# Optimization experiments

Measured on AMD Instinct MI355X. Metric: run time of the kernel, lower is better.

## Reference

```python
import jax, jax.numpy as jnp
import numpy as np

N_NODES = 50000
N_EDGES = 640000
HIDDEN = 128
NUM_GRAPHS = 50
EPS = 1e-5


def setup_inputs() -> dict:
    key = jax.random.key(0)
    k1, k2, k3, k4 = jax.random.split(key, 4)
    node = jax.random.normal(k1, (N_NODES, HIDDEN), dtype=jnp.float32)
    edge_index = jax.random.randint(k2, (2, N_EDGES), 0, N_NODES, dtype=jnp.int64)
    edge_attr = jax.random.uniform(k3, (N_EDGES,), dtype=jnp.float32)
    batch_ptr = jnp.sort(jax.random.randint(k4, (N_NODES,), 0, NUM_GRAPHS, dtype=jnp.int64))
    # GraphNorm learned params (init: weight=1, bias=0, mean_scale=1); perturb for a non-trivial test
    kw, kb, km = jax.random.split(jax.random.fold_in(key, 1), 3)
    weight = 1.0 + 0.1 * jax.random.normal(kw, (HIDDEN,), dtype=jnp.float32)
    bias = 0.1 * jax.random.normal(kb, (HIDDEN,), dtype=jnp.float32)
    mean_scale = 1.0 + 0.1 * jax.random.normal(km, (HIDDEN,), dtype=jnp.float32)
    return {"node": node, "edge_index": edge_index, "edge_attr": edge_attr,
            "batch_ptr": batch_ptr, "weight": weight, "bias": bias, "mean_scale": mean_scale}


def _segment_mean(x, seg, num_segments):
    s = jax.ops.segment_sum(x, seg, num_segments=num_segments)
    cnt = jax.ops.segment_sum(jnp.ones((x.shape[0], 1), x.dtype), seg, num_segments=num_segments)
    return s / jnp.maximum(cnt, 1.0)


def reference(node, edge_index, edge_attr, batch_ptr, weight, bias, mean_scale):
    n = node.shape[0]
    row, col = edge_index[0], edge_index[1]  # source -> target
    # gcn_norm (add_self_loops=False): symmetric normalization by target-degree
    deg = jax.ops.segment_sum(edge_attr, col, num_segments=n)
    dinv = jnp.where(deg > 0, deg ** -0.5, 0.0)
    norm_w = dinv[row] * edge_attr * dinv[col]  # [E]
    # LGConv propagate: scatter-add normalized source features to targets
    msg = node[row] * norm_w[:, None]            # [E, H]
    agg = jnp.zeros_like(node).at[col].add(msg)  # [N, H]
    # residual (skip_connection=True)
    h = node + agg
    # GraphNorm over per-graph segments
    mean = _segment_mean(h, batch_ptr, NUM_GRAPHS)            # [G, H]
    centered = h - mean[batch_ptr] * mean_scale               # [N, H]
    var = _segment_mean(centered * centered, batch_ptr, NUM_GRAPHS)
    out = centered / jnp.sqrt(var[batch_ptr] + EPS) * weight + bias
    return jax.nn.relu(out)
```

## Files before the change

kernel.cpp:

```cpp
#include <hip/hip_runtime.h>

#define N_NODES 50000
#define N_EDGES 640000
#define HIDDEN 128
#define NUM_GRAPHS 50
#define EPS 1e-5f
#define NBLK 196

#define CNT_SHIFT 44
#define FIX_MASK ((1ULL << CNT_SHIFT) - 1)
#define FIX_SCALE 4294967296.0f
#define FIX_INV (1.0f / 4294967296.0f)


__global__ void hist_kernel(const int* __restrict__ col, const float* __restrict__ ea,
                            unsigned long long* __restrict__ cnt64, int* __restrict__ rank) {
    int e = blockIdx.x * blockDim.x + threadIdx.x;
    if (e >= N_EDGES) return;
    int c = col[e];
    unsigned long long fx = (unsigned long long)(ea[e] * FIX_SCALE + 0.5f);
    unsigned long long old = atomicAdd(&cnt64[c], (1ULL << CNT_SHIFT) | fx);
    rank[e] = (int)(old >> CNT_SHIFT);
}

__global__ void scan1_kernel(const unsigned long long* __restrict__ cnt64,
                             int* __restrict__ bsum, float* __restrict__ dinv) {
    __shared__ int lds[256];
    int i = blockIdx.x * 256 + threadIdx.x;
    int c = 0;
    if (i < N_NODES) {
        unsigned long long v = cnt64[i];
        c = (int)(v >> CNT_SHIFT);
        unsigned long long lo = v & FIX_MASK;
        float deg = (float)lo * FIX_INV;
        dinv[i] = (lo != 0ULL) ? (1.0f / sqrtf(deg)) : 0.f;
    }
    lds[threadIdx.x] = c;
    __syncthreads();
    for (int off = 128; off > 0; off >>= 1) {
        if (threadIdx.x < off) lds[threadIdx.x] += lds[threadIdx.x + off];
        __syncthreads();
    }
    if (threadIdx.x == 0) bsum[blockIdx.x] = lds[0];
}

__global__ void scan2_kernel(const int* __restrict__ bsum, int* __restrict__ boff) {
    __shared__ int lds[256];
    int t = threadIdx.x;
    int v = (t < NBLK) ? bsum[t] : 0;
    lds[t] = v;
    __syncthreads();
    for (int off = 1; off < 256; off <<= 1) {
        int x = (t >= off) ? lds[t - off] : 0;
        __syncthreads();
        lds[t] += x;
        __syncthreads();
    }
    if (t < NBLK) boff[t] = lds[t] - v;
}

__global__ void scan3_kernel(const unsigned long long* __restrict__ cnt64,
                             const int* __restrict__ boff, int* __restrict__ rowptr) {
    __shared__ int lds[256];
    int i = blockIdx.x * 256 + threadIdx.x;
    int v = (i < N_NODES) ? (int)(cnt64[i] >> CNT_SHIFT) : 0;
    lds[threadIdx.x] = v;
    __syncthreads();
    for (int off = 1; off < 256; off <<= 1) {
        int x = (threadIdx.x >= off) ? lds[threadIdx.x - off] : 0;
        __syncthreads();
        lds[threadIdx.x] += x;
        __syncthreads();
    }
    if (i < N_NODES) rowptr[i] = boff[blockIdx.x] + lds[threadIdx.x] - v;
}

__global__ void place_kernel(const int* __restrict__ row, const int* __restrict__ col,
                             const float* __restrict__ ea, const float* __restrict__ rank,
                             const int* __restrict__ rowptr, const float* __restrict__ dinv,
                             int2* __restrict__ edat) {
    int e = blockIdx.x * blockDim.x + threadIdx.x;
    if (e >= N_EDGES) return;
    int r = row[e], c = col[e];
    float w = dinv[r] * ea[e];
    int pos = rowptr[c] + ((const int*)rank)[e];
    edat[pos] = make_int2(r, __float_as_int(w));
}

__global__ void gather_kernel(const int* __restrict__ rowptr,
                              const unsigned long long* __restrict__ cnt64,
                              const int2* __restrict__ edat, const float* __restrict__ dinv,
                              const float* __restrict__ node, float* __restrict__ out) {
    int n = blockIdx.x * 4 + (threadIdx.x >> 6);
    int lane = threadIdx.x & 63;
    if (n >= N_NODES) return;
    int j = rowptr[n];
    int end = j + (int)(cnt64[n] >> CNT_SHIFT);
    float dn = dinv[n];
    float2 a0 = {0.f, 0.f}, a1 = {0.f, 0.f}, a2 = {0.f, 0.f}, a3 = {0.f, 0.f};
    for (; j + 8 <= end; j += 8) {
        int2 e0 = edat[j + 0]; int2 e1 = edat[j + 1];
        int2 e2 = edat[j + 2]; int2 e3 = edat[j + 3];
        int2 e4 = edat[j + 4]; int2 e5 = edat[j + 5];
        int2 e6 = edat[j + 6]; int2 e7 = edat[j + 7];
        float2 v0 = ((const float2*)(node + (size_t)e0.x * HIDDEN))[lane];
        float2 v1 = ((const float2*)(node + (size_t)e1.x * HIDDEN))[lane];
        float2 v2 = ((const float2*)(node + (size_t)e2.x * HIDDEN))[lane];
        float2 v3 = ((const float2*)(node + (size_t)e3.x * HIDDEN))[lane];
        float2 v4 = ((const float2*)(node + (size_t)e4.x * HIDDEN))[lane];
        float2 v5 = ((const float2*)(node + (size_t)e5.x * HIDDEN))[lane];
        float2 v6 = ((const float2*)(node + (size_t)e6.x * HIDDEN))[lane];
        float2 v7 = ((const float2*)(node + (size_t)e7.x * HIDDEN))[lane];
        float w0 = __int_as_float(e0.y), w1 = __int_as_float(e1.y);
        float w2 = __int_as_float(e2.y), w3 = __int_as_float(e3.y);
        float w4 = __int_as_float(e4.y), w5 = __int_as_float(e5.y);
        float w6 = __int_as_float(e6.y), w7 = __int_as_float(e7.y);
        a0.x = fmaf(v0.x, w0, a0.x); a0.y = fmaf(v0.y, w0, a0.y);
        a1.x = fmaf(v1.x, w1, a1.x); a1.y = fmaf(v1.y, w1, a1.y);
        a2.x = fmaf(v2.x, w2, a2.x); a2.y = fmaf(v2.y, w2, a2.y);
        a3.x = fmaf(v3.x, w3, a3.x); a3.y = fmaf(v3.y, w3, a3.y);
        a0.x = fmaf(v4.x, w4, a0.x); a0.y = fmaf(v4.y, w4, a0.y);
        a1.x = fmaf(v5.x, w5, a1.x); a1.y = fmaf(v5.y, w5, a1.y);
        a2.x = fmaf(v6.x, w6, a2.x); a2.y = fmaf(v6.y, w6, a2.y);
        a3.x = fmaf(v7.x, w7, a3.x); a3.y = fmaf(v7.y, w7, a3.y);
    }
    for (; j < end; ++j) {
        int2 e = edat[j];
        float w = __int_as_float(e.y);
        float2 v = ((const float2*)(node + (size_t)e.x * HIDDEN))[lane];
        a0.x = fmaf(v.x, w, a0.x); a0.y = fmaf(v.y, w, a0.y);
    }
    float2 base = ((const float2*)(node + (size_t)n * HIDDEN))[lane];
    float sx = base.x + dn * ((a0.x + a1.x) + (a2.x + a3.x));
    float sy = base.y + dn * ((a0.y + a1.y) + (a2.y + a3.y));
    ((float2*)(out + (size_t)n * HIDDEN))[lane] = make_float2(sx, sy);
}


__global__ void stats_kernel(const float* __restrict__ h, const int* __restrict__ batch,
                             float* __restrict__ sum, float* __restrict__ sumsq) {
    int sub = threadIdx.x >> 5;
    int c4 = (threadIdx.x & 31) << 2;
    int i0 = blockIdx.x * 64;
    float4 s = make_float4(0.f, 0.f, 0.f, 0.f);
    float4 ss = make_float4(0.f, 0.f, 0.f, 0.f);
    int gcur = -1;
    for (int k = 0; k < 8; ++k) {
        int i = i0 + k * 8 + sub;
        if (i >= N_NODES) break;
        int g = batch[i];
        if (g != gcur) {
            if (gcur >= 0) {
                float* sp = &sum[gcur * HIDDEN + c4];
                atomicAdd(sp + 0, s.x); atomicAdd(sp + 1, s.y);
                atomicAdd(sp + 2, s.z); atomicAdd(sp + 3, s.w);
                float* qp = &sumsq[gcur * HIDDEN + c4];
                atomicAdd(qp + 0, ss.x); atomicAdd(qp + 1, ss.y);
                atomicAdd(qp + 2, ss.z); atomicAdd(qp + 3, ss.w);
            }
            gcur = g;
            s = make_float4(0.f, 0.f, 0.f, 0.f);
            ss = make_float4(0.f, 0.f, 0.f, 0.f);
        }
        float4 v = *(const float4*)(h + (size_t)i * HIDDEN + c4);
        s.x += v.x; s.y += v.y; s.z += v.z; s.w += v.w;
        ss.x += v.x * v.x; ss.y += v.y * v.y; ss.z += v.z * v.z; ss.w += v.w * v.w;
    }
    if (gcur >= 0) {
        float* sp = &sum[gcur * HIDDEN + c4];
        atomicAdd(sp + 0, s.x); atomicAdd(sp + 1, s.y);
        atomicAdd(sp + 2, s.z); atomicAdd(sp + 3, s.w);
        float* qp = &sumsq[gcur * HIDDEN + c4];
        atomicAdd(qp + 0, ss.x); atomicAdd(qp + 1, ss.y);
        atomicAdd(qp + 2, ss.z); atomicAdd(qp + 3, ss.w);
    }
}

__global__ void finalize_kernel(const float* __restrict__ sum, const float* __restrict__ sumsq,
                                const int* __restrict__ batch,
                                const float* __restrict__ mean_scale,
                                const float* __restrict__ weight,
                                float* __restrict__ msc, float* __restrict__ scale) {
    int t = blockIdx.x * blockDim.x + threadIdx.x;
    if (t >= NUM_GRAPHS * HIDDEN) return;
    int g = t >> 7;
    int c = t & 127;
    int lo0 = 0, hi0 = N_NODES;
    while (lo0 < hi0) { int m = (lo0 + hi0) >> 1; if (batch[m] < g) lo0 = m + 1; else hi0 = m; }
    int lo1 = lo0, hi1 = N_NODES;
    while (lo1 < hi1) { int m = (lo1 + hi1) >> 1; if (batch[m] < g + 1) lo1 = m + 1; else hi1 = m; }
    float n = fmaxf((float)(lo1 - lo0), 1.0f);
    float mean = sum[t] / n;
    float m2 = sumsq[t] / n;
    float ms = mean * mean_scale[c];
    float var = m2 - 2.f * ms * mean + ms * ms;
    msc[t] = ms;
    scale[t] = weight[c] / sqrtf(var + EPS);
}

__global__ void norm_kernel(float* __restrict__ out, const int* __restrict__ batch,
                            const float* __restrict__ msc, const float* __restrict__ scale,
                            const float* __restrict__ bias) {
    int t = blockIdx.x * blockDim.x + threadIdx.x;
    if (t >= N_NODES * HIDDEN / 4) return;
    int node_i = t >> 5;
    int c4 = (t & 31) << 2;
    int g = batch[node_i];
    float4 h = ((const float4*)out)[t];
    float4 m = *(const float4*)&msc[g * HIDDEN + c4];
    float4 sc = *(const float4*)&scale[g * HIDDEN + c4];
    float4 b = *(const float4*)&bias[c4];
    float4 o;
    o.x = fmaxf((h.x - m.x) * sc.x + b.x, 0.f);
    o.y = fmaxf((h.y - m.y) * sc.y + b.y, 0.f);
    o.z = fmaxf((h.z - m.z) * sc.z + b.z, 0.f);
    o.w = fmaxf((h.w - m.w) * sc.w + b.w, 0.f);
    ((float4*)out)[t] = o;
}


__global__ void deg_kernel(const int* __restrict__ col, const float* __restrict__ ea,
                           float* __restrict__ deg) {
    int e = blockIdx.x * blockDim.x + threadIdx.x;
    if (e < N_EDGES) atomicAdd(&deg[col[e]], ea[e]);
}

__global__ void dinv_kernel(float* __restrict__ deg) {
    int i = blockIdx.x * blockDim.x + threadIdx.x;
    if (i < N_NODES) {
        float d = deg[i];
        deg[i] = (d > 0.f) ? (1.0f / sqrtf(d)) : 0.f;
    }
}

__global__ void scatter_kernel(const int* __restrict__ row, const int* __restrict__ col,
                               const float* __restrict__ ea, const float* __restrict__ dinv,
                               const float* __restrict__ node, float* __restrict__ out) {
    int idx = blockIdx.x * blockDim.x + threadIdx.x;
    int e = idx >> 6;
    int lane = idx & 63;
    if (e >= N_EDGES) return;
    int r = row[e];
    int c = col[e];
    float w = dinv[r] * ea[e] * dinv[c];
    const float* src = node + (size_t)r * HIDDEN;
    float* dst = out + (size_t)c * HIDDEN;
    atomicAdd(&dst[lane], src[lane] * w);
    atomicAdd(&dst[lane + 64], src[lane + 64] * w);
}


extern "C" void kernel_launch(void* const* d_in, const int* in_sizes, int n_in,
                              void* d_out, int out_size, void* d_ws, size_t ws_size,
                              hipStream_t stream) {
    const float* node       = (const float*)d_in[0];
    const int*   eidx       = (const int*)d_in[1];
    const float* ea         = (const float*)d_in[2];
    const int*   batch      = (const int*)d_in[3];
    const float* weight     = (const float*)d_in[4];
    const float* bias       = (const float*)d_in[5];
    const float* mean_scale = (const float*)d_in[6];
    float* out = (float*)d_out;

    const int* row = eidx;
    const int* col = eidx + N_EDGES;

    char* wsb = (char*)d_ws;
    unsigned long long* cnt64 = (unsigned long long*)wsb;
    float* sum    = (float*)(cnt64 + 50048);
    float* sumsq  = sum + 6400;
    float* dinv   = sumsq + 6400;
    int*   rank   = (int*)(dinv + 50048);
    int*   rowptr = rank + N_EDGES;
    int2*  edat   = (int2*)(rowptr + 50048);
    float* msc    = (float*)(edat + N_EDGES);
    float* scale  = msc + 6400;
    int*   bsum   = (int*)(scale + 6400);
    int*   boff   = bsum + 256;
    size_t need = (size_t)((char*)(boff + 256) - wsb);

    if (ws_size >= need) {
        hipMemsetAsync(d_ws, 0, 50048 * 8 + 6400 * 2 * 4, stream);

        hist_kernel<<<(N_EDGES + 255) / 256, 256, 0, stream>>>(col, ea, cnt64, rank);
        scan1_kernel<<<NBLK, 256, 0, stream>>>(cnt64, bsum, dinv);
        scan2_kernel<<<1, 256, 0, stream>>>(bsum, boff);
        scan3_kernel<<<NBLK, 256, 0, stream>>>(cnt64, boff, rowptr);
        place_kernel<<<(N_EDGES + 255) / 256, 256, 0, stream>>>(
            row, col, ea, (const float*)rank, rowptr, dinv, edat);
        gather_kernel<<<(N_NODES + 3) / 4, 256, 0, stream>>>(
            rowptr, cnt64, edat, dinv, node, out);
    } else {
        float* f_deg   = (float*)wsb;
        float* f_sum   = f_deg + 50048;
        float* f_sumsq = f_sum + 6400;
        float* f_msc   = f_sumsq + 6400;
        float* f_scale = f_msc + 6400;
        sum = f_sum; sumsq = f_sumsq; msc = f_msc; scale = f_scale;

        hipMemsetAsync(d_ws, 0, (50048 + 6400 * 2) * sizeof(float), stream);
        hipMemcpyAsync(d_out, node, (size_t)N_NODES * HIDDEN * sizeof(float),
                       hipMemcpyDeviceToDevice, stream);
        deg_kernel<<<(N_EDGES + 255) / 256, 256, 0, stream>>>(col, ea, f_deg);
        dinv_kernel<<<(N_NODES + 255) / 256, 256, 0, stream>>>(f_deg);
        long long st = (long long)N_EDGES * 64;
        scatter_kernel<<<(int)((st + 255) / 256), 256, 0, stream>>>(row, col, ea, f_deg, node, out);
    }

    stats_kernel<<<(N_NODES + 63) / 64, 256, 0, stream>>>(out, batch, sum, sumsq);
    finalize_kernel<<<(NUM_GRAPHS * HIDDEN + 255) / 256, 256, 0, stream>>>(
        sum, sumsq, batch, mean_scale, weight, msc, scale);
    norm_kernel<<<(N_NODES * HIDDEN / 4 + 255) / 256, 256, 0, stream>>>(
        out, batch, msc, scale, bias);
}
```

Measured before the change: 255.7 us.

## Gather bf16 pre-scaled node features with padded CSR segments and merged scan

Adds a conversion kernel that pre-multiplies node features by dinv and packs them as bf16, so the gather reads half as many bytes per neighbour row. CSR segments are padded to multiples of 8 with zeroed slots, which removes the gather's scalar tail loop. The single-block scan2 kernel is folded into scan3. In exchange there is an extra full pass over node features, a larger memset of the padded edge buffer, and bf16 rounding error in the aggregated messages.

```diff
diff --git a/kernel.cpp b/kernel.cpp
--- a/kernel.cpp
+++ b/kernel.cpp
@@ -11,6 +11,13 @@
 #define FIX_MASK ((1ULL << CNT_SHIFT) - 1)
 #define FIX_SCALE 4294967296.0f
 #define FIX_INV (1.0f / 4294967296.0f)
+#define PAD8(c) (((c) + 7) & ~7)
+#define EDAT_SLOTS 990208
+
+__device__ __forceinline__ unsigned int bf16_rne(float f) {
+    unsigned int u = __float_as_uint(f);
+    return (u + 0x7FFFu + ((u >> 16) & 1u)) >> 16;
+}
 
 
 __global__ void hist_kernel(const int* __restrict__ col, const float* __restrict__ ea,
@@ -27,15 +34,16 @@
                              int* __restrict__ bsum, float* __restrict__ dinv) {
     __shared__ int lds[256];
     int i = blockIdx.x * 256 + threadIdx.x;
-    int c = 0;
+    int pc = 0;
     if (i < N_NODES) {
         unsigned long long v = cnt64[i];
-        c = (int)(v >> CNT_SHIFT);
+        int c = (int)(v >> CNT_SHIFT);
+        pc = PAD8(c);
         unsigned long long lo = v & FIX_MASK;
         float deg = (float)lo * FIX_INV;
         dinv[i] = (lo != 0ULL) ? (1.0f / sqrtf(deg)) : 0.f;
     }
-    lds[threadIdx.x] = c;
+    lds[threadIdx.x] = pc;
     __syncthreads();
     for (int off = 128; off > 0; off >>= 1) {
         if (threadIdx.x < off) lds[threadIdx.x] += lds[threadIdx.x + off];
@@ -44,10 +52,24 @@
     if (threadIdx.x == 0) bsum[blockIdx.x] = lds[0];
 }
 
-__global__ void scan2_kernel(const int* __restrict__ bsum, int* __restrict__ boff) {
+__global__ void scan3_kernel(const unsigned long long* __restrict__ cnt64,
+                             const int* __restrict__ bsum, int* __restrict__ rowptr) {
     __shared__ int lds[256];
+    __shared__ int base_s;
     int t = threadIdx.x;
-    int v = (t < NBLK) ? bsum[t] : 0;
+    int b = (t < (int)blockIdx.x && t < NBLK) ? bsum[t] : 0;
+    lds[t] = b;
+    __syncthreads();
+    for (int off = 128; off > 0; off >>= 1) {
+        if (t < off) lds[t] += lds[t + off];
+        __syncthreads();
+    }
+    if (t == 0) base_s = lds[0];
+    __syncthreads();
+    int base = base_s;
+    __syncthreads();
+    int i = blockIdx.x * 256 + t;
+    int v = (i < N_NODES) ? PAD8((int)(cnt64[i] >> CNT_SHIFT)) : 0;
     lds[t] = v;
     __syncthreads();
     for (int off = 1; off < 256; off <<= 1) {
@@ -56,79 +78,77 @@
         lds[t] += x;
         __syncthreads();
     }
-    if (t < NBLK) boff[t] = lds[t] - v;
-}
-
-__global__ void scan3_kernel(const unsigned long long* __restrict__ cnt64,
-                             const int* __restrict__ boff, int* __restrict__ rowptr) {
-    __shared__ int lds[256];
-    int i = blockIdx.x * 256 + threadIdx.x;
-    int v = (i < N_NODES) ? (int)(cnt64[i] >> CNT_SHIFT) : 0;
-    lds[threadIdx.x] = v;
-    __syncthreads();
-    for (int off = 1; off < 256; off <<= 1) {
-        int x = (threadIdx.x >= off) ? lds[threadIdx.x - off] : 0;
-        __syncthreads();
-        lds[threadIdx.x] += x;
-        __syncthreads();
-    }
-    if (i < N_NODES) rowptr[i] = boff[blockIdx.x] + lds[threadIdx.x] - v;
+    if (i < N_NODES) rowptr[i] = base + lds[t] - v;
+}
+
+__global__ void convert_kernel(const float* __restrict__ node, const float* __restrict__ dinv,
+                               unsigned int* __restrict__ snode) {
+    int t = blockIdx.x * blockDim.x + threadIdx.x;
+    if (t >= N_NODES * 64) return;
+    int n = t >> 6;
+    float d = dinv[n];
+    float2 v = ((const float2*)node)[t];
+    unsigned int lo = bf16_rne(v.x * d);
+    unsigned int hi = bf16_rne(v.y * d);
+    snode[t] = lo | (hi << 16);
 }
 
 __global__ void place_kernel(const int* __restrict__ row, const int* __restrict__ col,
-                             const float* __restrict__ ea, const float* __restrict__ rank,
-                             const int* __restrict__ rowptr, const float* __restrict__ dinv,
-                             int2* __restrict__ edat) {
+                             const float* __restrict__ ea, const int* __restrict__ rank,
+                             const int* __restrict__ rowptr, int2* __restrict__ edat) {
     int e = blockIdx.x * blockDim.x + threadIdx.x;
     if (e >= N_EDGES) return;
     int r = row[e], c = col[e];
-    float w = dinv[r] * ea[e];
-    int pos = rowptr[c] + ((const int*)rank)[e];
-    edat[pos] = make_int2(r, __float_as_int(w));
+    int pos = rowptr[c] + rank[e];
+    edat[pos] = make_int2(r, __float_as_int(ea[e]));
 }
 
 __global__ void gather_kernel(const int* __restrict__ rowptr,
                               const unsigned long long* __restrict__ cnt64,
                               const int2* __restrict__ edat, const float* __restrict__ dinv,
+                              const unsigned int* __restrict__ snode,
                               const float* __restrict__ node, float* __restrict__ out) {
     int n = blockIdx.x * 4 + (threadIdx.x >> 6);
     int lane = threadIdx.x & 63;
     if (n >= N_NODES) return;
+    int cnt = (int)(cnt64[n] >> CNT_SHIFT);
+    int iters = (cnt + 7) >> 3;
     int j = rowptr[n];
-    int end = j + (int)(cnt64[n] >> CNT_SHIFT);
     float dn = dinv[n];
     float2 a0 = {0.f, 0.f}, a1 = {0.f, 0.f}, a2 = {0.f, 0.f}, a3 = {0.f, 0.f};
-    for (; j + 8 <= end; j += 8) {
+    for (int it = 0; it < iters; ++it, j += 8) {
         int2 e0 = edat[j + 0]; int2 e1 = edat[j + 1];
         int2 e2 = edat[j + 2]; int2 e3 = edat[j + 3];
         int2 e4 = edat[j + 4]; int2 e5 = edat[j + 5];
         int2 e6 = edat[j + 6]; int2 e7 = edat[j + 7];
-        float2 v0 = ((const float2*)(node + (size_t)e0.x * HIDDEN))[lane];
-        float2 v1 = ((const float2*)(node + (size_t)e1.x * HIDDEN))[lane];
-        float2 v2 = ((const float2*)(node + (size_t)e2.x * HIDDEN))[lane];
-        float2 v3 = ((const float2*)(node + (size_t)e3.x * HIDDEN))[lane];
-        float2 v4 = ((const float2*)(node + (size_t)e4.x * HIDDEN))[lane];
-        float2 v5 = ((const float2*)(node + (size_t)e5.x * HIDDEN))[lane];
-        float2 v6 = ((const float2*)(node + (size_t)e6.x * HIDDEN))[lane];
-        float2 v7 = ((const float2*)(node + (size_t)e7.x * HIDDEN))[lane];
+        unsigned int p0 = snode[(size_t)e0.x * 64 + lane];
+        unsigned int p1 = snode[(size_t)e1.x * 64 + lane];
+        unsigned int p2 = snode[(size_t)e2.x * 64 + lane];
+        unsigned int p3 = snode[(size_t)e3.x * 64 + lane];
+        unsigned int p4 = snode[(size_t)e4.x * 64 + lane];
+        unsigned int p5 = snode[(size_t)e5.x * 64 + lane];
+        unsigned int p6 = snode[(size_t)e6.x * 64 + lane];
+        unsigned int p7 = snode[(size_t)e7.x * 64 + lane];
         float w0 = __int_as_float(e0.y), w1 = __int_as_float(e1.y);
         float w2 = __int_as_float(e2.y), w3 = __int_as_float(e3.y);
         float w4 = __int_as_float(e4.y), w5 = __int_as_float(e5.y);
         float w6 = __int_as_float(e6.y), w7 = __int_as_float(e7.y);
-        a0.x = fmaf(v0.x, w0, a0.x); a0.y = fmaf(v0.y, w0, a0.y);
-        a1.x = fmaf(v1.x, w1, a1.x); a1.y = fmaf(v1.y, w1, a1.y);
-        a2.x = fmaf(v2.x, w2, a2.x); a2.y = fmaf(v2.y, w2, a2.y);
-        a3.x = fmaf(v3.x, w3, a3.x); a3.y = fmaf(v3.y, w3, a3.y);
-        a0.x = fmaf(v4.x, w4, a0.x); a0.y = fmaf(v4.y, w4, a0.y);
-        a1.x = fmaf(v5.x, w5, a1.x); a1.y = fmaf(v5.y, w5, a1.y);
-        a2.x = fmaf(v6.x, w6, a2.x); a2.y = fmaf(v6.y, w6, a2.y);
-        a3.x = fmaf(v7.x, w7, a3.x); a3.y = fmaf(v7.y, w7, a3.y);
-    }
-    for (; j < end; ++j) {
-        int2 e = edat[j];
-        float w = __int_as_float(e.y);
-        float2 v = ((const float2*)(node + (size_t)e.x * HIDDEN))[lane];
-        a0.x = fmaf(v.x, w, a0.x); a0.y = fmaf(v.y, w, a0.y);
+        a0.x = fmaf(__uint_as_float(p0 << 16), w0, a0.x);
+        a0.y = fmaf(__uint_as_float(p0 & 0xFFFF0000u), w0, a0.y);
+        a1.x = fmaf(__uint_as_float(p1 << 16), w1, a1.x);
+        a1.y = fmaf(__uint_as_float(p1 & 0xFFFF0000u), w1, a1.y);
+        a2.x = fmaf(__uint_as_float(p2 << 16), w2, a2.x);
+        a2.y = fmaf(__uint_as_float(p2 & 0xFFFF0000u), w2, a2.y);
+        a3.x = fmaf(__uint_as_float(p3 << 16), w3, a3.x);
+        a3.y = fmaf(__uint_as_float(p3 & 0xFFFF0000u), w3, a3.y);
+        a0.x = fmaf(__uint_as_float(p4 << 16), w4, a0.x);
+        a0.y = fmaf(__uint_as_float(p4 & 0xFFFF0000u), w4, a0.y);
+        a1.x = fmaf(__uint_as_float(p5 << 16), w5, a1.x);
+        a1.y = fmaf(__uint_as_float(p5 & 0xFFFF0000u), w5, a1.y);
+        a2.x = fmaf(__uint_as_float(p6 << 16), w6, a2.x);
+        a2.y = fmaf(__uint_as_float(p6 & 0xFFFF0000u), w6, a2.y);
+        a3.x = fmaf(__uint_as_float(p7 << 16), w7, a3.x);
+        a3.y = fmaf(__uint_as_float(p7 & 0xFFFF0000u), w7, a3.y);
     }
     float2 base = ((const float2*)(node + (size_t)n * HIDDEN))[lane];
     float sx = base.x + dn * ((a0.x + a1.x) + (a2.x + a3.x));
@@ -269,27 +289,27 @@
     unsigned long long* cnt64 = (unsigned long long*)wsb;
     float* sum    = (float*)(cnt64 + 50048);
     float* sumsq  = sum + 6400;
-    float* dinv   = sumsq + 6400;
+    int2*  edat   = (int2*)(sumsq + 6400);
+    float* dinv   = (float*)(edat + EDAT_SLOTS);
     int*   rank   = (int*)(dinv + 50048);
     int*   rowptr = rank + N_EDGES;
-    int2*  edat   = (int2*)(rowptr + 50048);
-    float* msc    = (float*)(edat + N_EDGES);
+    unsigned int* snode = (unsigned int*)(rowptr + 50048);
+    float* msc    = (float*)(snode + 3200000);
     float* scale  = msc + 6400;
     int*   bsum   = (int*)(scale + 6400);
-    int*   boff   = bsum + 256;
-    size_t need = (size_t)((char*)(boff + 256) - wsb);
+    size_t need = (size_t)((char*)(bsum + 256) - wsb);
+    size_t zero_bytes = 50048 * 8 + 6400 * 2 * 4 + (size_t)EDAT_SLOTS * 8;
 
     if (ws_size >= need) {
-        hipMemsetAsync(d_ws, 0, 50048 * 8 + 6400 * 2 * 4, stream);
+        hipMemsetAsync(d_ws, 0, zero_bytes, stream);
 
         hist_kernel<<<(N_EDGES + 255) / 256, 256, 0, stream>>>(col, ea, cnt64, rank);
         scan1_kernel<<<NBLK, 256, 0, stream>>>(cnt64, bsum, dinv);
-        scan2_kernel<<<1, 256, 0, stream>>>(bsum, boff);
-        scan3_kernel<<<NBLK, 256, 0, stream>>>(cnt64, boff, rowptr);
-        place_kernel<<<(N_EDGES + 255) / 256, 256, 0, stream>>>(
-            row, col, ea, (const float*)rank, rowptr, dinv, edat);
+        scan3_kernel<<<NBLK, 256, 0, stream>>>(cnt64, bsum, rowptr);
+        convert_kernel<<<(N_NODES * 64 + 255) / 256, 256, 0, stream>>>(node, dinv, snode);
+        place_kernel<<<(N_EDGES + 255) / 256, 256, 0, stream>>>(row, col, ea, rank, rowptr, edat);
         gather_kernel<<<(N_NODES + 3) / 4, 256, 0, stream>>>(
-            rowptr, cnt64, edat, dinv, node, out);
+            rowptr, cnt64, edat, dinv, snode, node, out);
     } else {
         float* f_deg   = (float*)wsb;
         float* f_sum   = f_deg + 50048;
```

Result: faster. 240.5 us (-5.9%).
